# Kernel tuning notes

Measured on AMD Instinct MI355X. Metric: run time of the kernel, lower is better.

The kernel has to match this reference:

```python
import jax, jax.numpy as jnp
import numpy as np

D_MODEL = 1024
N_HEADS = 16
D_FF = 4096
EPS = 1e-6


def layernorm(x, alpha, bias):
    # torch.std uses Bessel correction (ddof=1)
    mean = jnp.mean(x, axis=-1, keepdims=True)
    std = jnp.std(x, axis=-1, keepdims=True, ddof=1)
    return alpha * (x - mean) / (std + EPS) + bias


def setup_inputs() -> dict:
    key = jax.random.key(0)
    ks = jax.random.split(key, 12)
    s = 1.0 / np.sqrt(D_MODEL)
    sf = 1.0 / np.sqrt(D_FF)
    return {
        "x": jax.random.normal(ks[0], (2, 2048, D_MODEL), jnp.float32),
        "mask": jnp.ones((2, 1, 1, 2048), jnp.int32),
        "wq": jax.random.normal(ks[1], (D_MODEL, D_MODEL), jnp.float32) * s,
        "wk": jax.random.normal(ks[2], (D_MODEL, D_MODEL), jnp.float32) * s,
        "wv": jax.random.normal(ks[3], (D_MODEL, D_MODEL), jnp.float32) * s,
        "wo": jax.random.normal(ks[4], (D_MODEL, D_MODEL), jnp.float32) * s,
        "wo_b": jnp.zeros((D_MODEL,), jnp.float32),
        "w1": jax.random.normal(ks[5], (D_MODEL, D_FF), jnp.float32) * s,
        "b1": jnp.zeros((D_FF,), jnp.float32),
        "w2": jax.random.normal(ks[6], (D_FF, D_MODEL), jnp.float32) * sf,
        "b2": jnp.zeros((D_MODEL,), jnp.float32),
        "alpha1": jnp.ones((D_MODEL,), jnp.float32),
        "bias1": jnp.zeros((D_MODEL,), jnp.float32),
        "alpha2": jnp.ones((D_MODEL,), jnp.float32),
        "bias2": jnp.zeros((D_MODEL,), jnp.float32),
    }


def reference(x, mask, wq, wk, wv, wo, wo_b, w1, b1, w2, b2,
              alpha1, bias1, alpha2, bias2):
    B, S, D = x.shape
    h, dk = N_HEADS, D_MODEL // N_HEADS
    # projections -> [B, h, S, dk]
    q = (x @ wq).reshape(B, S, h, dk).transpose(0, 2, 1, 3)
    k = (x @ wk).reshape(B, S, h, dk).transpose(0, 2, 1, 3)
    v = (x @ wv).reshape(B, S, h, dk).transpose(0, 2, 1, 3)
    scores = jnp.einsum('bhqd,bhkd->bhqk', q, k) / jnp.sqrt(jnp.float32(dk))
    scores = jnp.where(mask == 0, jnp.float32(-1e9), scores)
    attn = jax.nn.softmax(scores, axis=-1)
    ctx = jnp.einsum('bhqk,bhkd->bhqd', attn, v)
    ctx = ctx.transpose(0, 2, 1, 3).reshape(B, S, D)
    attn_out = ctx @ wo + wo_b
    x = layernorm(x + attn_out, alpha1, bias1)
    ff = jax.nn.relu(x @ w1 + b1) @ w2 + b2
    x = layernorm(x + ff, alpha2, bias2)
    return x
```

## Files before the change

kernel.cpp:

```cpp
#include <hip/hip_runtime.h>
#include <hip/hip_bf16.h>

#define D_MODEL 1024
#define N_HEADS 16
#define DK      64
#define SEQ     2048
#define BATCH   2
#define D_FF    4096
#define ROWS    (BATCH*SEQ)
#define LN_EPS  1e-6f
#define SSTR    72
#define KTILE   128
#define PSTR    136

typedef __hip_bfloat16 bf16;
typedef __attribute__((ext_vector_type(8))) short frag8;
typedef __attribute__((ext_vector_type(4))) float facc4;

__device__ inline float bf2f(unsigned short u){ return __uint_as_float(((unsigned)u) << 16); }
__device__ inline float toF(bf16 v){ return __bfloat162float(v); }
__device__ inline unsigned short f2bu(float f){ bf16 h = __float2bfloat16(f); return *reinterpret_cast<unsigned short*>(&h); }

__device__ inline float ld1(const void* p, size_t idx, bool f32) {
    return f32 ? ((const float*)p)[idx] : toF(((const bf16*)p)[idx]);
}

struct U8 { unsigned short v[8]; };
__device__ inline U8 ld8bf(const void* p, size_t idx, bool f32) {
    U8 r;
    if (!f32) {
        *reinterpret_cast<uint4*>(r.v) = *reinterpret_cast<const uint4*>((const unsigned short*)p + idx);
    } else {
        const float* f = (const float*)p + idx;
        const float4 a = *reinterpret_cast<const float4*>(f);
        const float4 b = *reinterpret_cast<const float4*>(f + 4);
        r.v[0]=f2bu(a.x); r.v[1]=f2bu(a.y); r.v[2]=f2bu(a.z); r.v[3]=f2bu(a.w);
        r.v[4]=f2bu(b.x); r.v[5]=f2bu(b.y); r.v[6]=f2bu(b.z); r.v[7]=f2bu(b.w);
    }
    return r;
}

__device__ inline void gld16(const void* g, void* l) {
    __builtin_amdgcn_global_load_lds(
        reinterpret_cast<const __attribute__((address_space(1))) void*>(
            reinterpret_cast<uintptr_t>(g)),
        reinterpret_cast<__attribute__((address_space(3))) void*>(
            (unsigned int)reinterpret_cast<uintptr_t>(l)),
        16, 0, 0);
}

__global__ void probe_kernel(const void* __restrict__ xp, int* __restrict__ flag) {
    __shared__ int hit;
    if (threadIdx.x == 0) hit = 0;
    __syncthreads();
    const bf16* p = (const bf16*)xp;
    int bad = 0;
    for (int i = threadIdx.x; i < 8192; i += 256) {
        float v = fabsf(toF(p[i]));
        if (!(v <= 1e5f)) bad = 1;
    }
    if (bad) atomicOr(&hit, 1);
    __syncthreads();
    if (threadIdx.x == 0) *flag = hit;
}

__global__ __launch_bounds__(256) void xcvt_kernel(const void* __restrict__ x,
    bf16* __restrict__ out, const int* __restrict__ flagp)
{
    const bool f32 = (*flagp) != 0;
    const size_t i = ((size_t)blockIdx.x * 256 + threadIdx.x) * 8;
    U8 d = ld8bf(x, i, f32);
    *reinterpret_cast<uint4*>(out + i) = *reinterpret_cast<const uint4*>(d.v);
}

__global__ __launch_bounds__(256) void transpose_kernel(const void* __restrict__ W,
    bf16* __restrict__ WT, int K, int N, const int* __restrict__ flagp)
{
    const bool f32 = (*flagp) != 0;
    __shared__ float tile[32][33];
    const int tx = threadIdx.x, ty = threadIdx.y;
    const int n0 = blockIdx.x * 32, k0 = blockIdx.y * 32;
    #pragma unroll
    for (int r = 0; r < 4; ++r)
        tile[ty + 8*r][tx] = ld1(W, (size_t)(k0 + ty + 8*r) * N + n0 + tx, f32);
    __syncthreads();
    #pragma unroll
    for (int r = 0; r < 4; ++r)
        WT[(size_t)(n0 + ty + 8*r) * K + k0 + tx] = __float2bfloat16(tile[tx][ty + 8*r]);
}

__global__ __launch_bounds__(256) void transpose4_kernel(const void* __restrict__ w0,
    const void* __restrict__ w1, const void* __restrict__ w2, const void* __restrict__ w3,
    bf16* __restrict__ WT4, const int* __restrict__ flagp)
{
    const bool f32 = (*flagp) != 0;
    const int which = blockIdx.z;
    const void* W = (which == 0) ? w0 : (which == 1) ? w1 : (which == 2) ? w2 : w3;
    bf16* WT = WT4 + (size_t)which * D_MODEL * D_MODEL;
    __shared__ float tile[32][33];
    const int tx = threadIdx.x, ty = threadIdx.y;
    const int n0 = blockIdx.x * 32, k0 = blockIdx.y * 32;
    #pragma unroll
    for (int r = 0; r < 4; ++r)
        tile[ty + 8*r][tx] = ld1(W, (size_t)(k0 + ty + 8*r) * D_MODEL + n0 + tx, f32);
    __syncthreads();
    #pragma unroll
    for (int r = 0; r < 4; ++r)
        WT[(size_t)(n0 + ty + 8*r) * D_MODEL + k0 + tx] = __float2bfloat16(tile[tx][ty + 8*r]);
}

__global__ __launch_bounds__(256) void vtrans_kernel(const bf16* __restrict__ V,
    bf16* __restrict__ VT)
{
    __shared__ unsigned short tile[32][33];
    const int tx = threadIdx.x, ty = threadIdx.y;
    const int s0 = blockIdx.x * 32, d0 = blockIdx.y * 32;
    const int bh = blockIdx.z, b = bh >> 4, h = bh & 15;
    #pragma unroll
    for (int r = 0; r < 4; ++r)
        tile[ty + 8*r][tx] = *reinterpret_cast<const unsigned short*>(
            V + ((size_t)(b * SEQ + s0 + ty + 8*r)) * D_MODEL + h * DK + d0 + tx);
    __syncthreads();
    #pragma unroll
    for (int r = 0; r < 4; ++r)
        *reinterpret_cast<unsigned short*>(
            VT + ((size_t)(bh * DK + d0 + ty + 8*r)) * SEQ + s0 + tx) = tile[tx][ty + 8*r];
}

template<bool RELU, bool BIAS, int NMAT, int SPLITK>
__global__ __launch_bounds__(256) void mgemm_kernel(const bf16* __restrict__ A,
    const bf16* __restrict__ BT, const void* __restrict__ bias,
    bf16* __restrict__ C, int M, int N, int K, const int* __restrict__ flagp)
{
    const bool inF32 = (*flagp) != 0;

    __shared__ unsigned short sA[128 * 64];
    __shared__ unsigned short sB[128 * 64];

    int which = 0, colb = blockIdx.x;
    if (NMAT > 1) { which = blockIdx.x >> 3; colb = blockIdx.x & 7; }
    const int kslice = (SPLITK > 1) ? blockIdx.z : 0;
    const int Kspan  = K / SPLITK;
    const int kbase  = kslice * Kspan;
    const bf16* Bp = BT + (size_t)which * N * K;
    bf16*       Cp = C  + (size_t)which * M * N + (size_t)kslice * M * N;

    const int row0 = blockIdx.y * 128;
    const int col0 = colb * 128;

    const int t    = threadIdx.x;
    const int wave = t >> 6;
    const int lane = t & 63;
    const int lm   = lane & 15;
    const int q    = lane >> 4;
    const int wm   = (wave & 1) * 64;
    const int wn   = (wave >> 1) * 64;

    facc4 acc[4][4];
    #pragma unroll
    for (int i = 0; i < 4; ++i)
        #pragma unroll
        for (int j = 0; j < 4; ++j)
            acc[i][j] = (facc4){0.f, 0.f, 0.f, 0.f};

    for (int k0 = kbase; k0 < kbase + Kspan; k0 += 64) {
        __syncthreads();
        #pragma unroll
        for (int j = 0; j < 4; ++j) {
            const int ch = (wave * 4 + j) * 64 + lane;
            const int r  = ch >> 3;
            const int cs = ch & 7;
            const int c  = cs ^ (r & 7);
            gld16(A  + (size_t)(row0 + r) * K + k0 + 8 * c, &sA[(wave * 4 + j) * 512]);
            gld16(Bp + (size_t)(col0 + r) * K + k0 + 8 * c, &sB[(wave * 4 + j) * 512]);
        }
        __syncthreads();

        #pragma unroll
        for (int kk = 0; kk < 64; kk += 32) {
            const int cr = (kk >> 3) + q;
            frag8 af[4], bfr[4];
            #pragma unroll
            for (int im = 0; im < 4; ++im) {
                const int m = wm + 16 * im + lm;
                af[im] = *reinterpret_cast<const frag8*>(&sA[m * 64 + ((cr ^ (m & 7)) << 3)]);
            }
            #pragma unroll
            for (int in = 0; in < 4; ++in) {
                const int n = wn + 16 * in + lm;
                bfr[in] = *reinterpret_cast<const frag8*>(&sB[n * 64 + ((cr ^ (n & 7)) << 3)]);
            }
            #pragma unroll
            for (int im = 0; im < 4; ++im)
                #pragma unroll
                for (int in = 0; in < 4; ++in)
                    acc[im][in] = __builtin_amdgcn_mfma_f32_16x16x32_bf16(af[im], bfr[in], acc[im][in], 0, 0, 0);
        }
    }

    #pragma unroll
    for (int in = 0; in < 4; ++in) {
        const int col = col0 + wn + 16*in + lm;
        float bv = 0.f;
        if (BIAS && kslice == 0) bv = ld1(bias, col, inF32);
        #pragma unroll
        for (int im = 0; im < 4; ++im) {
            #pragma unroll
            for (int r = 0; r < 4; ++r) {
                const int row = row0 + wm + 16*im + 4*q + r;
                float v = acc[im][in][r] + bv;
                if (RELU) v = fmaxf(v, 0.f);
                Cp[(size_t)row * N + col] = __float2bfloat16(v);
            }
        }
    }
}

__global__ __launch_bounds__(512) void fattn_kernel(
    const bf16* __restrict__ Qg, const bf16* __restrict__ Kg,
    const bf16* __restrict__ VTg, const int* __restrict__ mask,
    bf16* __restrict__ ctx)
{
    __shared__ unsigned short sK[128 * 64];
    __shared__ unsigned short sV[64 * 128];
    __shared__ unsigned short PsU[8 * 16 * PSTR];
    __shared__ float madd[KTILE];

    const int t    = threadIdx.x;
    const int qt   = blockIdx.x;
    const int h    = blockIdx.y;
    const int b    = blockIdx.z;
    const int q0   = qt * 128;
    const int bh   = b * N_HEADS + h;
    const int wave = t >> 6;
    const int lane = t & 63;
    const int lm   = lane & 15;
    const int qd   = lane >> 4;

    unsigned short* Qs = PsU;
    {
        const int sr = t >> 2, sd0 = (t & 3) * 16;
        const unsigned short* src = (const unsigned short*)
            (Qg + ((size_t)(b * SEQ + q0 + sr)) * D_MODEL + h * DK + sd0);
        unsigned short qi[16], qo[16];
        *reinterpret_cast<uint4*>(&qi[0]) = *reinterpret_cast<const uint4*>(src);
        *reinterpret_cast<uint4*>(&qi[8]) = *reinterpret_cast<const uint4*>(src + 8);
        #pragma unroll
        for (int u = 0; u < 16; ++u) qo[u] = f2bu(bf2f(qi[u]) * 0.125f);
        *reinterpret_cast<uint4*>(&Qs[sr * SSTR + sd0])     = *reinterpret_cast<const uint4*>(&qo[0]);
        *reinterpret_cast<uint4*>(&Qs[sr * SSTR + sd0 + 8]) = *reinterpret_cast<const uint4*>(&qo[8]);
    }
    __syncthreads();
    frag8 qf[2];
    #pragma unroll
    for (int s2 = 0; s2 < 2; ++s2)
        qf[s2] = *reinterpret_cast<const frag8*>(&Qs[(16 * wave + lm) * SSTR + 32 * s2 + 8 * qd]);

    facc4 accO[4];
    float m_r[4], l_r[4];
    #pragma unroll
    for (int r = 0; r < 4; ++r) { m_r[r] = -1e30f; l_r[r] = 0.f; }
    #pragma unroll
    for (int in = 0; in < 4; ++in) accO[in] = (facc4){0.f, 0.f, 0.f, 0.f};

    for (int kt = 0; kt < SEQ / KTILE; ++kt) {
        const int k0 = kt * KTILE;
        __syncthreads();

        #pragma unroll
        for (int j = 0; j < 2; ++j) {
            const int ch = (wave * 2 + j) * 64 + lane;
            const int rK = ch >> 3, cK = (ch & 7) ^ (rK & 7);
            gld16(Kg + ((size_t)(b * SEQ + k0 + rK)) * D_MODEL + h * DK + 8 * cK,
                  &sK[(wave * 2 + j) * 512]);
            const int rV = ch >> 4, cV = (ch & 15) ^ (rV & 15);
            gld16(VTg + ((size_t)(bh * DK + rV)) * SEQ + k0 + 8 * cV,
                  &sV[(wave * 2 + j) * 512]);
        }
        if (t < KTILE) madd[t] = (mask[b * SEQ + k0 + t] == 0) ? -1e9f : 0.f;
        __syncthreads();

        facc4 accS[8];
        #pragma unroll
        for (int i = 0; i < 8; ++i) accS[i] = (facc4){0.f, 0.f, 0.f, 0.f};
        #pragma unroll
        for (int i = 0; i < 8; ++i) {
            #pragma unroll
            for (int s2 = 0; s2 < 2; ++s2) {
                const int cr = 4 * s2 + qd;
                frag8 kf = *reinterpret_cast<const frag8*>(
                    &sK[(16 * i + lm) * 64 + ((cr ^ (lm & 7)) << 3)]);
                accS[i] = __builtin_amdgcn_mfma_f32_16x16x32_bf16(qf[s2], kf, accS[i], 0, 0, 0);
            }
        }

        float madv[8];
        #pragma unroll
        for (int i = 0; i < 8; ++i) madv[i] = madd[16 * i + lm];

        float mx[4];
        #pragma unroll
        for (int r = 0; r < 4; ++r) {
            float m0 = -1e30f;
            #pragma unroll
            for (int i = 0; i < 8; ++i) m0 = fmaxf(m0, accS[i][r] + madv[i]);
            #pragma unroll
            for (int off = 1; off < 16; off <<= 1) m0 = fmaxf(m0, __shfl_xor(m0, off));
            mx[r] = m0;
        }

        float alpha[4], mn[4], psum[4];
        #pragma unroll
        for (int r = 0; r < 4; ++r) {
            mn[r] = fmaxf(m_r[r], mx[r]);
            alpha[r] = __expf(m_r[r] - mn[r]);
            m_r[r] = mn[r];
            psum[r] = 0.f;
        }
        unsigned short* Pw = &PsU[wave * 16 * PSTR];
        #pragma unroll
        for (int i = 0; i < 8; ++i) {
            #pragma unroll
            for (int r = 0; r < 4; ++r) {
                float p = __expf(accS[i][r] + madv[i] - mn[r]);
                psum[r] += p;
                Pw[(qd * 4 + r) * PSTR + 16 * i + lm] = f2bu(p);
            }
        }
        #pragma unroll
        for (int r = 0; r < 4; ++r) {
            float s = psum[r];
            #pragma unroll
            for (int off = 1; off < 16; off <<= 1) s += __shfl_xor(s, off);
            l_r[r] = l_r[r] * alpha[r] + s;
            #pragma unroll
            for (int in = 0; in < 4; ++in) accO[in][r] *= alpha[r];
        }

        #pragma unroll
        for (int c = 0; c < 4; ++c) {
            frag8 pf = *reinterpret_cast<const frag8*>(&Pw[lm * PSTR + 32 * c + 8 * qd]);
            #pragma unroll
            for (int in = 0; in < 4; ++in) {
                const int cr = 4 * c + qd;
                frag8 vf = *reinterpret_cast<const frag8*>(
                    &sV[(16 * in + lm) * 128 + ((cr ^ lm) << 3)]);
                accO[in] = __builtin_amdgcn_mfma_f32_16x16x32_bf16(pf, vf, accO[in], 0, 0, 0);
            }
        }
    }

    float inv[4];
    #pragma unroll
    for (int r = 0; r < 4; ++r) inv[r] = 1.f / l_r[r];
    #pragma unroll
    for (int in = 0; in < 4; ++in)
        #pragma unroll
        for (int r = 0; r < 4; ++r)
            ctx[((size_t)(b * SEQ + q0 + 16 * wave + qd * 4 + r)) * D_MODEL + h * DK + 16 * in + lm]
                = __float2bfloat16(accO[in][r] * inv[r]);
}

template<bool BASE_WS, bool OUT_WS>
__global__ __launch_bounds__(256) void ln_kernel(const void* __restrict__ base,
    const bf16* __restrict__ addv, const bf16* __restrict__ addv2,
    const void* __restrict__ alpha, const void* __restrict__ bias,
    void* __restrict__ outp, const int* __restrict__ flagp)
{
    const bool inF32 = (*flagp) != 0;
    __shared__ float vals[D_MODEL];
    __shared__ float red[256];
    const int row = blockIdx.x, tid = threadIdx.x;

    float lsum = 0.f;
    for (int i = tid; i < D_MODEL; i += 256) {
        const size_t off = (size_t)row * D_MODEL + i;
        float v = (BASE_WS ? toF(((const bf16*)base)[off]) : ld1(base, off, inF32)) + toF(addv[off]);
        if (addv2) v += toF(addv2[off]);
        vals[i] = v; lsum += v;
    }
    red[tid] = lsum; __syncthreads();
    for (int s = 128; s > 0; s >>= 1) { if (tid < s) red[tid] += red[tid + s]; __syncthreads(); }
    const float mean = red[0] / (float)D_MODEL; __syncthreads();

    float lsq = 0.f;
    for (int i = tid; i < D_MODEL; i += 256) { float dd = vals[i] - mean; lsq += dd * dd; }
    red[tid] = lsq; __syncthreads();
    for (int s = 128; s > 0; s >>= 1) { if (tid < s) red[tid] += red[tid + s]; __syncthreads(); }
    const float var = red[0] / (float)(D_MODEL - 1);
    const float inv = 1.f / (sqrtf(var) + LN_EPS);

    for (int i = tid; i < D_MODEL; i += 256) {
        const size_t off = (size_t)row * D_MODEL + i;
        const float y = ld1(alpha, i, inF32) * (vals[i] - mean) * inv + ld1(bias, i, inF32);
        if (OUT_WS || !inF32) ((bf16*)outp)[off] = __float2bfloat16(y);
        else                  ((float*)outp)[off] = y;
    }
}

extern "C" void kernel_launch(void* const* d_in, const int* in_sizes, int n_in,
                              void* d_out, int out_size, void* d_ws, size_t ws_size,
                              hipStream_t stream)
{
    const void* x    = d_in[0];
    const int*  mask = (const int*)d_in[1];
    const void* wq   = d_in[2];
    const void* wk   = d_in[3];
    const void* wv   = d_in[4];
    const void* wo   = d_in[5];
    const void* wo_b = d_in[6];
    const void* w1   = d_in[7];
    const void* b1   = d_in[8];
    const void* w2   = d_in[9];
    const void* b2   = d_in[10];
    const void* al1  = d_in[11];
    const void* bi1  = d_in[12];
    const void* al2  = d_in[13];
    const void* bi2  = d_in[14];

    const size_t MB = 1024 * 1024;
    char* ws = (char*)d_ws;
    const bool BIG = ws_size >= 64 * MB + 4096;
    if (!BIG && ws_size < 56 * MB + 4096) return;

    dim3 tb(32, 8);

    if (BIG) {
        bf16* Qb   = (bf16*)(ws + 0 * MB);
        bf16* Kb   = (bf16*)(ws + 8 * MB);
        bf16* Vb   = (bf16*)(ws + 16 * MB);
        bf16* Xb   = (bf16*)(ws + 24 * MB);
        bf16* VTb  = (bf16*)(ws + 24 * MB);
        bf16* WT4  = (bf16*)(ws + 32 * MB);
        bf16* WOT  = WT4 + (size_t)3 * D_MODEL * D_MODEL;
        bf16* W1T  = (bf16*)(ws + 40 * MB);
        bf16* W2T  = (bf16*)(ws + 48 * MB);
        bf16* CTXb = (bf16*)(ws + 56 * MB);
        bf16* ATT0 = (bf16*)(ws + 0 * MB);
        bf16* ATT1 = (bf16*)(ws + 8 * MB);
        bf16* X1b  = (bf16*)(ws + 56 * MB);
        bf16* FFb  = (bf16*)(ws + 0 * MB);
        bf16* X20  = (bf16*)(ws + 32 * MB);
        bf16* X21  = (bf16*)(ws + 40 * MB);
        int*  flagp = (int*)(ws + 64 * MB);

        probe_kernel<<<1, 256, 0, stream>>>(x, flagp);
        xcvt_kernel<<<dim3(ROWS * D_MODEL / 2048), 256, 0, stream>>>(x, Xb, flagp);

        transpose4_kernel<<<dim3(32, 32, 4), tb, 0, stream>>>(wq, wk, wv, wo, WT4, flagp);
        transpose_kernel<<<dim3(128, 32), tb, 0, stream>>>(w1, W1T, D_MODEL, D_FF, flagp);
        transpose_kernel<<<dim3(32, 128), tb, 0, stream>>>(w2, W2T, D_FF, D_MODEL, flagp);

        mgemm_kernel<false, false, 3, 1><<<dim3(24, 32), 256, 0, stream>>>(
            Xb, WT4, nullptr, Qb, ROWS, D_MODEL, D_MODEL, flagp);

        vtrans_kernel<<<dim3(SEQ / 32, 2, BATCH * N_HEADS), tb, 0, stream>>>(Vb, VTb);

        fattn_kernel<<<dim3(SEQ / 128, N_HEADS, BATCH), 512, 0, stream>>>(Qb, Kb, VTb, mask, CTXb);

        mgemm_kernel<false, true, 1, 2><<<dim3(8, 32, 2), 256, 0, stream>>>(
            CTXb, WOT, wo_b, ATT0, ROWS, D_MODEL, D_MODEL, flagp);
        ln_kernel<false, true><<<ROWS, 256, 0, stream>>>(x, ATT0, ATT1, al1, bi1, X1b, flagp);

        mgemm_kernel<true, true, 1, 1><<<dim3(32, 32), 256, 0, stream>>>(
            X1b, W1T, b1, FFb, ROWS, D_FF, D_MODEL, flagp);

        mgemm_kernel<false, true, 1, 2><<<dim3(8, 32, 2), 256, 0, stream>>>(
            FFb, W2T, b2, X20, ROWS, D_MODEL, D_FF, flagp);
        ln_kernel<true, false><<<ROWS, 256, 0, stream>>>(X1b, X20, X21, al2, bi2, d_out, flagp);
    } else {
        bf16* Qb    = (bf16*)(ws + 0 * MB);
        bf16* Kb    = (bf16*)(ws + 8 * MB);
        bf16* Vb    = (bf16*)(ws + 16 * MB);
        bf16* Xb    = (bf16*)(ws + 24 * MB);
        bf16* VTb   = (bf16*)(ws + 24 * MB);
        bf16* WQKVT = (bf16*)(ws + 32 * MB);
        bf16* CTXb  = (bf16*)(ws + 32 * MB);
        bf16* W2T   = (bf16*)(ws + 32 * MB);
        bf16* WOT   = (bf16*)(ws + 0 * MB);
        bf16* ATT0  = (bf16*)(ws + 48 * MB);
        bf16* W1T   = (bf16*)(ws + 48 * MB);
        bf16* X20   = (bf16*)(ws + 48 * MB);
        bf16* X1b   = (bf16*)(ws + 40 * MB);
        bf16* FFb   = (bf16*)(ws + 0 * MB);
        int*  flagp = (int*)(ws + 56 * MB);

        probe_kernel<<<1, 256, 0, stream>>>(x, flagp);
        xcvt_kernel<<<dim3(ROWS * D_MODEL / 2048), 256, 0, stream>>>(x, Xb, flagp);

        transpose_kernel<<<dim3(32, 32), tb, 0, stream>>>(wq, WQKVT,           D_MODEL, D_MODEL, flagp);
        transpose_kernel<<<dim3(32, 32), tb, 0, stream>>>(wk, WQKVT + 1048576, D_MODEL, D_MODEL, flagp);
        transpose_kernel<<<dim3(32, 32), tb, 0, stream>>>(wv, WQKVT + 2097152, D_MODEL, D_MODEL, flagp);

        mgemm_kernel<false, false, 3, 1><<<dim3(24, 32), 256, 0, stream>>>(
            Xb, WQKVT, nullptr, Qb, ROWS, D_MODEL, D_MODEL, flagp);

        vtrans_kernel<<<dim3(SEQ / 32, 2, BATCH * N_HEADS), tb, 0, stream>>>(Vb, VTb);

        fattn_kernel<<<dim3(SEQ / 128, N_HEADS, BATCH), 512, 0, stream>>>(Qb, Kb, VTb, mask, CTXb);

        transpose_kernel<<<dim3(32, 32), tb, 0, stream>>>(wo, WOT, D_MODEL, D_MODEL, flagp);
        mgemm_kernel<false, true, 1, 1><<<dim3(8, 32), 256, 0, stream>>>(
            CTXb, WOT, wo_b, ATT0, ROWS, D_MODEL, D_MODEL, flagp);
        ln_kernel<false, true><<<ROWS, 256, 0, stream>>>(x, ATT0, nullptr, al1, bi1, X1b, flagp);

        transpose_kernel<<<dim3(128, 32), tb, 0, stream>>>(w1, W1T, D_MODEL, D_FF, flagp);
        mgemm_kernel<true, true, 1, 1><<<dim3(32, 32), 256, 0, stream>>>(
            X1b, W1T, b1, FFb, ROWS, D_FF, D_MODEL, flagp);

        transpose_kernel<<<dim3(32, 128), tb, 0, stream>>>(w2, W2T, D_FF, D_MODEL, flagp);
        mgemm_kernel<false, true, 1, 1><<<dim3(8, 32), 256, 0, stream>>>(
            FFb, W2T, b2, X20, ROWS, D_MODEL, D_FF, flagp);
        ln_kernel<true, false><<<ROWS, 256, 0, stream>>>(X1b, X20, nullptr, al2, bi2, d_out, flagp);
    }
}
```

Baseline: 397.0 us.

## Merge weight transposes, shrink attention key tile, use exp2, single-pass layernorm

Combines the six weight transposes into one launch indexed by a flat block id. Halves the flash-attention key tile to 64 with matching LDS buffers, and folds log2e into the Q scale so softmax can use the hardware exp2. Rewrites layernorm to load four elements per thread and compute sum and sum of squares in one reduction, dropping the shared value buffer and the second pass. The smaller tile adds loop iterations and barriers, and the one-pass variance is less numerically robust.

```diff
diff --git a/kernel.cpp b/kernel.cpp
--- a/kernel.cpp
+++ b/kernel.cpp
@@ -10,8 +10,7 @@
 #define ROWS    (BATCH*SEQ)
 #define LN_EPS  1e-6f
 #define SSTR    72
-#define KTILE   128
-#define PSTR    136
+#define LOG2E   1.4426950408889634f
 
 typedef __hip_bfloat16 bf16;
 typedef __attribute__((ext_vector_type(8))) short frag8;
@@ -23,6 +22,15 @@
 
 __device__ inline float ld1(const void* p, size_t idx, bool f32) {
     return f32 ? ((const float*)p)[idx] : toF(((const bf16*)p)[idx]);
+}
+__device__ inline void ld4f(const void* p, size_t idx, bool f32, float* o) {
+    if (f32) {
+        const float4 f = *reinterpret_cast<const float4*>((const float*)p + idx);
+        o[0] = f.x; o[1] = f.y; o[2] = f.z; o[3] = f.w;
+    } else {
+        const ushort4 u = *reinterpret_cast<const ushort4*>((const unsigned short*)p + idx);
+        o[0] = bf2f(u.x); o[1] = bf2f(u.y); o[2] = bf2f(u.z); o[3] = bf2f(u.w);
+    }
 }
 
 struct U8 { unsigned short v[8]; };
@@ -89,24 +97,37 @@
         WT[(size_t)(n0 + ty + 8*r) * K + k0 + tx] = __float2bfloat16(tile[tx][ty + 8*r]);
 }
 
-__global__ __launch_bounds__(256) void transpose4_kernel(const void* __restrict__ w0,
-    const void* __restrict__ w1, const void* __restrict__ w2, const void* __restrict__ w3,
-    bf16* __restrict__ WT4, const int* __restrict__ flagp)
+__global__ __launch_bounds__(256) void wtransall_kernel(const void* __restrict__ wq,
+    const void* __restrict__ wk, const void* __restrict__ wv, const void* __restrict__ wo,
+    const void* __restrict__ w1, const void* __restrict__ w2,
+    bf16* __restrict__ dst, const int* __restrict__ flagp)
 {
     const bool f32 = (*flagp) != 0;
-    const int which = blockIdx.z;
-    const void* W = (which == 0) ? w0 : (which == 1) ? w1 : (which == 2) ? w2 : w3;
-    bf16* WT = WT4 + (size_t)which * D_MODEL * D_MODEL;
+    const int id = blockIdx.x;
+    const void* W; bf16* WT; int K, N, n0, k0;
+    if (id < 4096) {
+        const int which = id >> 10, tid = id & 1023;
+        W = (which == 0) ? wq : (which == 1) ? wk : (which == 2) ? wv : wo;
+        WT = dst + (size_t)which * 1048576; K = 1024; N = 1024;
+        n0 = (tid & 31) * 32; k0 = (tid >> 5) * 32;
+    } else if (id < 8192) {
+        const int tid = id - 4096;
+        W = w1; WT = dst + 4194304; K = 1024; N = 4096;
+        n0 = (tid & 127) * 32; k0 = (tid >> 7) * 32;
+    } else {
+        const int tid = id - 8192;
+        W = w2; WT = dst + 8388608; K = 4096; N = 1024;
+        n0 = (tid & 31) * 32; k0 = (tid >> 5) * 32;
+    }
     __shared__ float tile[32][33];
     const int tx = threadIdx.x, ty = threadIdx.y;
-    const int n0 = blockIdx.x * 32, k0 = blockIdx.y * 32;
     #pragma unroll
     for (int r = 0; r < 4; ++r)
-        tile[ty + 8*r][tx] = ld1(W, (size_t)(k0 + ty + 8*r) * D_MODEL + n0 + tx, f32);
+        tile[ty + 8*r][tx] = ld1(W, (size_t)(k0 + ty + 8*r) * N + n0 + tx, f32);
     __syncthreads();
     #pragma unroll
     for (int r = 0; r < 4; ++r)
-        WT[(size_t)(n0 + ty + 8*r) * D_MODEL + k0 + tx] = __float2bfloat16(tile[tx][ty + 8*r]);
+        WT[(size_t)(n0 + ty + 8*r) * K + k0 + tx] = __float2bfloat16(tile[tx][ty + 8*r]);
 }
 
 __global__ __launch_bounds__(256) void vtrans_kernel(const bf16* __restrict__ V,
@@ -169,8 +190,7 @@
         for (int j = 0; j < 4; ++j) {
             const int ch = (wave * 4 + j) * 64 + lane;
             const int r  = ch >> 3;
-            const int cs = ch & 7;
-            const int c  = cs ^ (r & 7);
+            const int c  = (ch & 7) ^ (r & 7);
             gld16(A  + (size_t)(row0 + r) * K + k0 + 8 * c, &sA[(wave * 4 + j) * 512]);
             gld16(Bp + (size_t)(col0 + r) * K + k0 + 8 * c, &sB[(wave * 4 + j) * 512]);
         }
@@ -221,10 +241,10 @@
     const bf16* __restrict__ VTg, const int* __restrict__ mask,
     bf16* __restrict__ ctx)
 {
-    __shared__ unsigned short sK[128 * 64];
-    __shared__ unsigned short sV[64 * 128];
-    __shared__ unsigned short PsU[8 * 16 * PSTR];
-    __shared__ float madd[KTILE];
+    __shared__ unsigned short sK[64 * 64];
+    __shared__ unsigned short sV[64 * 64];
+    __shared__ unsigned short PsU[8 * 16 * SSTR];
+    __shared__ float madd[64];
 
     const int t    = threadIdx.x;
     const int qt   = blockIdx.x;
@@ -246,7 +266,7 @@
         *reinterpret_cast<uint4*>(&qi[0]) = *reinterpret_cast<const uint4*>(src);
         *reinterpret_cast<uint4*>(&qi[8]) = *reinterpret_cast<const uint4*>(src + 8);
         #pragma unroll
-        for (int u = 0; u < 16; ++u) qo[u] = f2bu(bf2f(qi[u]) * 0.125f);
+        for (int u = 0; u < 16; ++u) qo[u] = f2bu(bf2f(qi[u]) * (0.125f * LOG2E));
         *reinterpret_cast<uint4*>(&Qs[sr * SSTR + sd0])     = *reinterpret_cast<const uint4*>(&qo[0]);
         *reinterpret_cast<uint4*>(&Qs[sr * SSTR + sd0 + 8]) = *reinterpret_cast<const uint4*>(&qo[8]);
     }
@@ -263,28 +283,26 @@
     #pragma unroll
     for (int in = 0; in < 4; ++in) accO[in] = (facc4){0.f, 0.f, 0.f, 0.f};
 
-    for (int kt = 0; kt < SEQ / KTILE; ++kt) {
-        const int k0 = kt * KTILE;
+    for (int kt = 0; kt < SEQ / 64; ++kt) {
+        const int k0 = kt * 64;
         __syncthreads();
 
-        #pragma unroll
-        for (int j = 0; j < 2; ++j) {
-            const int ch = (wave * 2 + j) * 64 + lane;
-            const int rK = ch >> 3, cK = (ch & 7) ^ (rK & 7);
-            gld16(Kg + ((size_t)(b * SEQ + k0 + rK)) * D_MODEL + h * DK + 8 * cK,
-                  &sK[(wave * 2 + j) * 512]);
-            const int rV = ch >> 4, cV = (ch & 15) ^ (rV & 15);
-            gld16(VTg + ((size_t)(bh * DK + rV)) * SEQ + k0 + 8 * cV,
-                  &sV[(wave * 2 + j) * 512]);
-        }
-        if (t < KTILE) madd[t] = (mask[b * SEQ + k0 + t] == 0) ? -1e9f : 0.f;
+        {
+            const int r  = t >> 3;
+            const int c  = (t & 7) ^ (r & 7);
+            gld16(Kg + ((size_t)(b * SEQ + k0 + r)) * D_MODEL + h * DK + 8 * c,
+                  &sK[wave * 512]);
+            gld16(VTg + ((size_t)(bh * DK + r)) * SEQ + k0 + 8 * c,
+                  &sV[wave * 512]);
+        }
+        if (t < 64) madd[t] = (mask[b * SEQ + k0 + t] == 0) ? -1e9f : 0.f;
         __syncthreads();
 
-        facc4 accS[8];
-        #pragma unroll
-        for (int i = 0; i < 8; ++i) accS[i] = (facc4){0.f, 0.f, 0.f, 0.f};
-        #pragma unroll
-        for (int i = 0; i < 8; ++i) {
+        facc4 accS[4];
+        #pragma unroll
+        for (int i = 0; i < 4; ++i) accS[i] = (facc4){0.f, 0.f, 0.f, 0.f};
+        #pragma unroll
+        for (int i = 0; i < 4; ++i) {
             #pragma unroll
             for (int s2 = 0; s2 < 2; ++s2) {
                 const int cr = 4 * s2 + qd;
@@ -294,16 +312,16 @@
             }
         }
 
-        float madv[8];
-        #pragma unroll
-        for (int i = 0; i < 8; ++i) madv[i] = madd[16 * i + lm];
+        float madv[4];
+        #pragma unroll
+        for (int i = 0; i < 4; ++i) madv[i] = madd[16 * i + lm];
 
         float mx[4];
         #pragma unroll
         for (int r = 0; r < 4; ++r) {
             float m0 = -1e30f;
             #pragma unroll
-            for (int i = 0; i < 8; ++i) m0 = fmaxf(m0, accS[i][r] + madv[i]);
+            for (int i = 0; i < 4; ++i) m0 = fmaxf(m0, accS[i][r] + madv[i]);
             #pragma unroll
             for (int off = 1; off < 16; off <<= 1) m0 = fmaxf(m0, __shfl_xor(m0, off));
             mx[r] = m0;
@@ -313,18 +331,18 @@
         #pragma unroll
         for (int r = 0; r < 4; ++r) {
             mn[r] = fmaxf(m_r[r], mx[r]);
-            alpha[r] = __expf(m_r[r] - mn[r]);
+            alpha[r] = __builtin_amdgcn_exp2f(m_r[r] - mn[r]);
             m_r[r] = mn[r];
             psum[r] = 0.f;
         }
-        unsigned short* Pw = &PsU[wave * 16 * PSTR];
-        #pragma unroll
-        for (int i = 0; i < 8; ++i) {
+        unsigned short* Pw = &PsU[wave * 16 * SSTR];
+        #pragma unroll
+        for (int i = 0; i < 4; ++i) {
             #pragma unroll
             for (int r = 0; r < 4; ++r) {
-                float p = __expf(accS[i][r] + madv[i] - mn[r]);
+                float p = __builtin_amdgcn_exp2f(accS[i][r] + madv[i] - mn[r]);
                 psum[r] += p;
-                Pw[(qd * 4 + r) * PSTR + 16 * i + lm] = f2bu(p);
+                Pw[(qd * 4 + r) * SSTR + 16 * i + lm] = f2bu(p);
             }
         }
         #pragma unroll
@@ -338,13 +356,13 @@
         }
 
         #pragma unroll
-        for (int c = 0; c < 4; ++c) {
-            frag8 pf = *reinterpret_cast<const frag8*>(&Pw[lm * PSTR + 32 * c + 8 * qd]);
+        for (int c = 0; c < 2; ++c) {
+            frag8 pf = *reinterpret_cast<const frag8*>(&Pw[lm * SSTR + 32 * c + 8 * qd]);
             #pragma unroll
             for (int in = 0; in < 4; ++in) {
                 const int cr = 4 * c + qd;
                 frag8 vf = *reinterpret_cast<const frag8*>(
-                    &sV[(16 * in + lm) * 128 + ((cr ^ lm) << 3)]);
+                    &sV[(16 * in + lm) * 64 + ((cr ^ (lm & 7)) << 3)]);
                 accO[in] = __builtin_amdgcn_mfma_f32_16x16x32_bf16(pf, vf, accO[in], 0, 0, 0);
             }
         }
@@ -368,33 +386,48 @@
     void* __restrict__ outp, const int* __restrict__ flagp)
 {
     const bool inF32 = (*flagp) != 0;
-    __shared__ float vals[D_MODEL];
-    __shared__ float red[256];
+    __shared__ float2 red[256];
     const int row = blockIdx.x, tid = threadIdx.x;
-
-    float lsum = 0.f;
-    for (int i = tid; i < D_MODEL; i += 256) {
-        const size_t off = (size_t)row * D_MODEL + i;
-        float v = (BASE_WS ? toF(((const bf16*)base)[off]) : ld1(base, off, inF32)) + toF(addv[off]);
-        if (addv2) v += toF(addv2[off]);
-        vals[i] = v; lsum += v;
-    }
-    red[tid] = lsum; __syncthreads();
-    for (int s = 128; s > 0; s >>= 1) { if (tid < s) red[tid] += red[tid + s]; __syncthreads(); }
-    const float mean = red[0] / (float)D_MODEL; __syncthreads();
-
-    float lsq = 0.f;
-    for (int i = tid; i < D_MODEL; i += 256) { float dd = vals[i] - mean; lsq += dd * dd; }
-    red[tid] = lsq; __syncthreads();
-    for (int s = 128; s > 0; s >>= 1) { if (tid < s) red[tid] += red[tid + s]; __syncthreads(); }
-    const float var = red[0] / (float)(D_MODEL - 1);
-    const float inv = 1.f / (sqrtf(var) + LN_EPS);
-
-    for (int i = tid; i < D_MODEL; i += 256) {
-        const size_t off = (size_t)row * D_MODEL + i;
-        const float y = ld1(alpha, i, inF32) * (vals[i] - mean) * inv + ld1(bias, i, inF32);
-        if (OUT_WS || !inF32) ((bf16*)outp)[off] = __float2bfloat16(y);
-        else                  ((float*)outp)[off] = y;
+    const int i0 = 4 * tid;
+    const size_t off = (size_t)row * D_MODEL + i0;
+
+    float v[4];
+    if (BASE_WS) ld4f(base, off, false, v);
+    else         ld4f(base, off, inF32, v);
+    {
+        const ushort4 u = *reinterpret_cast<const ushort4*>((const unsigned short*)addv + off);
+        v[0] += bf2f(u.x); v[1] += bf2f(u.y); v[2] += bf2f(u.z); v[3] += bf2f(u.w);
+    }
+    if (addv2) {
+        const ushort4 u = *reinterpret_cast<const ushort4*>((const unsigned short*)addv2 + off);
+        v[0] += bf2f(u.x); v[1] += bf2f(u.y); v[2] += bf2f(u.z); v[3] += bf2f(u.w);
+    }
+
+    float s = v[0] + v[1] + v[2] + v[3];
+    float sq = v[0]*v[0] + v[1]*v[1] + v[2]*v[2] + v[3]*v[3];
+    red[tid] = make_float2(s, sq); __syncthreads();
+    for (int st = 128; st > 0; st >>= 1) {
+        if (tid < st) { red[tid].x += red[tid + st].x; red[tid].y += red[tid + st].y; }
+        __syncthreads();
+    }
+    const float S = red[0].x, SQ = red[0].y;
+    const float mean = S * (1.f / D_MODEL);
+    const float var  = (SQ - S * mean) * (1.f / (D_MODEL - 1));
+    const float inv  = 1.f / (sqrtf(var) + LN_EPS);
+
+    float la[4], lb[4];
+    ld4f(alpha, i0, inF32, la);
+    ld4f(bias,  i0, inF32, lb);
+    float y[4];
+    #pragma unroll
+    for (int j = 0; j < 4; ++j) y[j] = la[j] * (v[j] - mean) * inv + lb[j];
+
+    if (OUT_WS || !inF32) {
+        ushort4 o;
+        o.x = f2bu(y[0]); o.y = f2bu(y[1]); o.z = f2bu(y[2]); o.w = f2bu(y[3]);
+        *reinterpret_cast<ushort4*>((unsigned short*)outp + off) = o;
+    } else {
+        *reinterpret_cast<float4*>((float*)outp + off) = make_float4(y[0], y[1], y[2], y[3]);
     }
 }
 
@@ -447,9 +480,7 @@
         probe_kernel<<<1, 256, 0, stream>>>(x, flagp);
         xcvt_kernel<<<dim3(ROWS * D_MODEL / 2048), 256, 0, stream>>>(x, Xb, flagp);
 
-        transpose4_kernel<<<dim3(32, 32, 4), tb, 0, stream>>>(wq, wk, wv, wo, WT4, flagp);
-        transpose_kernel<<<dim3(128, 32), tb, 0, stream>>>(w1, W1T, D_MODEL, D_FF, flagp);
-        transpose_kernel<<<dim3(32, 128), tb, 0, stream>>>(w2, W2T, D_FF, D_MODEL, flagp);
+        wtransall_kernel<<<dim3(12288), tb, 0, stream>>>(wq, wk, wv, wo, w1, w2, WT4, flagp);
 
         mgemm_kernel<false, false, 3, 1><<<dim3(24, 32), 256, 0, stream>>>(
             Xb, WT4, nullptr, Qb, ROWS, D_MODEL, D_MODEL, flagp);
```

After: 427.4 us. 1.08x slower.
